# Kernel optimization log

Hardware: AMD Instinct MI355X
Metric: run time of the kernel (lower is better)

The kernel has to match this reference:

```python
import jax, jax.numpy as jnp
import numpy as np

V = 50257   # vocab
P = 2048    # max positions
D = 768     # hidden
H = 12      # heads
F = 3072    # 4*D ffn
NL = 12     # layers
L = 2048    # seq len
EPS = 1e-5


def setup_inputs() -> dict:
    key = jax.random.key(0)
    ks = jax.random.split(key, 12)
    r = lambda k, shp: jax.random.normal(k, shp, jnp.float32) * 0.02
    return dict(
        input_ids=jax.random.randint(ks[0], (1, L), 0, V, dtype=jnp.int32),
        attention_mask=jnp.ones((1, L), jnp.int32),
        wte=r(ks[1], (V, D)),
        wpe=r(ks[2], (P, D)),
        lnf_w=jnp.ones((D,), jnp.float32),
        lnf_b=jnp.zeros((D,), jnp.float32),
        ln1_w=jnp.ones((NL, D), jnp.float32),
        ln1_b=jnp.zeros((NL, D), jnp.float32),
        qw=r(ks[3], (NL, D, D)),
        kw=r(ks[4], (NL, D, D)),
        vw=r(ks[5], (NL, D, D)),
        ow=r(ks[6], (NL, D, D)),
        ob=jnp.zeros((NL, D), jnp.float32),
        ln2_w=jnp.ones((NL, D), jnp.float32),
        ln2_b=jnp.zeros((NL, D), jnp.float32),
        fcw=r(ks[7], (NL, D, F)),
        fcb=jnp.zeros((NL, F), jnp.float32),
        pw=r(ks[8], (NL, F, D)),
        pb=jnp.zeros((NL, D), jnp.float32),
    )


def _ln(x, w, b):
    mu = jnp.mean(x, -1, keepdims=True)
    var = jnp.mean((x - mu) ** 2, -1, keepdims=True)
    return (x - mu) * jax.lax.rsqrt(var + EPS) * w + b


def reference(input_ids, attention_mask, wte, wpe, lnf_w, lnf_b,
              ln1_w, ln1_b, qw, kw, vw, ow, ob, ln2_w, ln2_b,
              fcw, fcb, pw, pb):
    ids = input_ids.reshape(-1, input_ids.shape[-1])          # [1, L]
    pos = jnp.cumsum(attention_mask, -1) - 1
    pos = jnp.where(attention_mask == 0, 1, pos)
    h = (wte[ids] + wpe[pos])[0]                               # [L, D]

    key_valid = attention_mask[0] > 0                          # actual_length mask
    mask = jnp.tril(jnp.ones((L, L), bool)) & key_valid[None, :]  # causal+pad
    dh = D // H

    def layer(h, p):
        l1w, l1b, Wq, Wk, Wv, Wo, bo, l2w, l2b, Wf, bf, Wp, bp = p
        x = _ln(h, l1w, l1b)
        q = (x @ Wq).reshape(L, H, dh)
        k = (x @ Wk).reshape(L, H, dh)
        v = (x @ Wv).reshape(L, H, dh)
        # GPT-Neo attention: NO 1/sqrt(dh) scaling
        scores = jnp.einsum('qhd,khd->hqk', q, k)
        scores = jnp.where(mask[None], scores, jnp.float32(-1e9))
        attn = jax.nn.softmax(scores, axis=-1)
        ctx = jnp.einsum('hqk,khd->qhd', attn, v).reshape(L, D)
        h = h + ctx @ Wo + bo
        y = _ln(h, l2w, l2b)
        h = h + jax.nn.gelu(y @ Wf + bf, approximate=True) @ Wp + bp
        return h, None

    h, _ = jax.lax.scan(layer, h, (ln1_w, ln1_b, qw, kw, vw, ow, ob,
                                   ln2_w, ln2_b, fcw, fcb, pw, pb))
    return _ln(h[None, :, :], lnf_w, lnf_b)                    # [1, L, D]
```

## Files before the change

kernel.cpp:

```cpp
#include <hip/hip_runtime.h>
#include <hip/hip_bf16.h>
#include <math.h>
#include <stdint.h>

#define L 2048
#define D 768
#define H 12
#define DH 64
#define F 3072
#define NL 12
#define QKVN 2304

typedef __attribute__((ext_vector_type(8))) short bf16x8;
typedef __attribute__((ext_vector_type(4))) float f32x4;

__device__ __forceinline__ ushort f2bf(float x) {
    union { float f; uint32_t u; } c; c.f = x;
    uint32_t r = c.u + 0x7FFFu + ((c.u >> 16) & 1u);
    return (ushort)(r >> 16);
}

__device__ __forceinline__ uint32_t cvt_pk_bf16(float lo, float hi) {
    uint32_t r;
    asm("v_cvt_pk_bf16_f32 %0, %1, %2" : "=v"(r) : "v"(lo), "v"(hi));
    return r;
}

__device__ __forceinline__ bf16x8 ldfrag(const ushort* p) {
    ushort4 lo = *(const ushort4*)(p);
    ushort4 hi = *(const ushort4*)(p + 16);
    bf16x8 f;
    f[0] = (short)lo.x; f[1] = (short)lo.y; f[2] = (short)lo.z; f[3] = (short)lo.w;
    f[4] = (short)hi.x; f[5] = (short)hi.y; f[6] = (short)hi.z; f[7] = (short)hi.w;
    return f;
}

__device__ __forceinline__ float gelu_tanh(float x) {
    float c = 0.7978845608028654f;
    float inner = c * (x + 0.044715f * x * x * x);
    return 0.5f * x * (1.0f + tanhf(inner));
}

__global__ void pos_kernel(const int* __restrict__ mask, int* __restrict__ pos) {
    __shared__ int sm[L];
    for (int i = threadIdx.x; i < L; i += blockDim.x) sm[i] = mask[i];
    __syncthreads();
    int t = blockIdx.x * blockDim.x + threadIdx.x;
    if (t < L) {
        int s = 0;
        for (int j = 0; j <= t; ++j) s += sm[j];
        int p = s - 1;
        if (sm[t] == 0) p = 1;
        pos[t] = p;
    }
}

__global__ void maskb_kernel(const int* __restrict__ mask, float* __restrict__ mb) {
    int i = blockIdx.x * blockDim.x + threadIdx.x;
    if (i < L) mb[i] = mask[i] ? 0.f : -1e9f;
}

__global__ __launch_bounds__(256) void embed_kernel(const int* __restrict__ ids,
                                                    const int* __restrict__ pos,
                                                    const float* __restrict__ wte,
                                                    const float* __restrict__ wpe,
                                                    float* __restrict__ h) {
    int t = blockIdx.x;
    int id = ids[t];
    int p = pos[t];
    const float* we = wte + (size_t)id * D;
    const float* wp = wpe + (size_t)p * D;
    float* hr = h + (size_t)t * D;
#pragma unroll
    for (int i = 0; i < 3; ++i) {
        int d = threadIdx.x + i * 256;
        hr[d] = we[d] + wp[d];
    }
}

template <bool OUTBF>
__global__ __launch_bounds__(256) void ln_kernel(const float* __restrict__ in,
                                                 const float* __restrict__ w,
                                                 const float* __restrict__ b,
                                                 float* __restrict__ outF,
                                                 ushort* __restrict__ outB) {
    __shared__ float red[2][4];
    int row = blockIdx.x;
    const float* x = in + (size_t)row * D;
    int t = threadIdx.x;
    float v0 = x[t], v1 = x[t + 256], v2 = x[t + 512];
    float s = v0 + v1 + v2;
    float ss = v0 * v0 + v1 * v1 + v2 * v2;
#pragma unroll
    for (int o = 32; o; o >>= 1) {
        s += __shfl_xor(s, o);
        ss += __shfl_xor(ss, o);
    }
    int wave = t >> 6;
    if ((t & 63) == 0) { red[0][wave] = s; red[1][wave] = ss; }
    __syncthreads();
    s = red[0][0] + red[0][1] + red[0][2] + red[0][3];
    ss = red[1][0] + red[1][1] + red[1][2] + red[1][3];
    float mean = s * (1.f / D);
    float var = ss * (1.f / D) - mean * mean;
    float rstd = rsqrtf(var + 1e-5f);
#pragma unroll
    for (int i = 0; i < 3; ++i) {
        int d = t + i * 256;
        float vv = (i == 0) ? v0 : (i == 1) ? v1 : v2;
        float y = (vv - mean) * rstd * w[d] + b[d];
        if (OUTBF) outB[(size_t)row * D + d] = f2bf(y);
        else       outF[(size_t)row * D + d] = y;
    }
}

template <int S, bool OUTBF>
__global__ __launch_bounds__(256) void redln_kernel(const float* __restrict__ part,
                                                    const float* __restrict__ bias,
                                                    float* __restrict__ h,
                                                    const float* __restrict__ lnw,
                                                    const float* __restrict__ lnb,
                                                    ushort* __restrict__ outB,
                                                    float* __restrict__ outF) {
    __shared__ float red[2][4];
    int row = blockIdx.x;
    int t = threadIdx.x;
    float v[3];
    float s = 0.f, ss = 0.f;
#pragma unroll
    for (int i = 0; i < 3; ++i) {
        int d = t + i * 256;
        float x = h[(size_t)row * D + d] + bias[d];
#pragma unroll
        for (int sp = 0; sp < S; ++sp)
            x += part[((size_t)sp * L + row) * D + d];
        v[i] = x;
        h[(size_t)row * D + d] = x;
        s += x;
        ss += x * x;
    }
#pragma unroll
    for (int o = 32; o; o >>= 1) {
        s += __shfl_xor(s, o);
        ss += __shfl_xor(ss, o);
    }
    int wave = t >> 6;
    if ((t & 63) == 0) { red[0][wave] = s; red[1][wave] = ss; }
    __syncthreads();
    s = red[0][0] + red[0][1] + red[0][2] + red[0][3];
    ss = red[1][0] + red[1][1] + red[1][2] + red[1][3];
    float mean = s * (1.f / D);
    float var = ss * (1.f / D) - mean * mean;
    float rstd = rsqrtf(var + 1e-5f);
#pragma unroll
    for (int i = 0; i < 3; ++i) {
        int d = t + i * 256;
        float y = (v[i] - mean) * rstd * lnw[d] + lnb[d];
        if (OUTBF) outB[(size_t)row * D + d] = f2bf(y);
        else       outF[(size_t)row * D + d] = y;
    }
}

__global__ __launch_bounds__(256) void tcast_f32(const float* __restrict__ in,
                                                 ushort* __restrict__ out,
                                                 int K, int N,
                                                 size_t inStride, size_t outStride) {
    in += blockIdx.z * inStride;
    out += blockIdx.z * outStride;
    __shared__ float tile[64][65];
    int k0 = blockIdx.y * 64, n0 = blockIdx.x * 64;
    int t = threadIdx.x;
    int cl = t & 63, rg = t >> 6;
#pragma unroll
    for (int i = 0; i < 16; ++i) {
        int r = rg + 4 * i;
        tile[r][cl] = in[(size_t)(k0 + r) * N + n0 + cl];
    }
    __syncthreads();
#pragma unroll
    for (int i = 0; i < 16; ++i) {
        int r = rg + 4 * i;
        out[(size_t)(n0 + r) * K + k0 + cl] = f2bf(tile[cl][r]);
    }
}

template <int ACT, bool OUTBF, int SPLITK, bool VSPLIT>
__global__ __launch_bounds__(256) void gemm_bf16(const ushort* __restrict__ A,
                                                 const ushort* __restrict__ Bt,
                                                 const float* __restrict__ bias,
                                                 const float* __restrict__ resid,
                                                 float* __restrict__ outF,
                                                 ushort* __restrict__ outB,
                                                 float* __restrict__ pout,
                                                 ushort* __restrict__ vTout,
                                                 int M, int N, int K) {
    __shared__ __align__(16) char lds[32768];
    const int tid = threadIdx.x;
    const int lane = tid & 63, w = tid >> 6;
    const int wr = w >> 1, wc = w & 1;
    const int bm = blockIdx.y * 128, bn = blockIdx.x * 128;
    const int l15 = lane & 15, l4 = lane >> 4;
    const int srow = tid >> 2, c = tid & 3;
    const int blo = (c & 1) * 32 + (c >> 1) * 8;
    const int kLen = K / SPLITK;
    const int kStart = (SPLITK > 1) ? blockIdx.z * kLen : 0;

    const int sxor = (srow & 3) << 4;
    const int wo0 = srow * 64 + (blo ^ sxor);
    const int wo1 = srow * 64 + ((blo + 16) ^ sxor);
    const int rxor = (l4 * 16) ^ ((l15 & 3) << 4);
    const int aBase = (wr * 64 + l15) * 64 + rxor;
    const int bBase = (wc * 64 + l15) * 64 + rxor;

    f32x4 acc[4][4];
#pragma unroll
    for (int m = 0; m < 4; ++m)
#pragma unroll
        for (int n = 0; n < 4; ++n)
            acc[m][n] = (f32x4){0.f, 0.f, 0.f, 0.f};

    const ushort* Ag = A + (size_t)(bm + srow) * K + kStart + c * 8;
    const ushort* Ag2 = Ag + (size_t)64 * K;
    const ushort* Bg = Bt + (size_t)(bn + srow) * K + kStart + c * 8;
    const ushort* Bg2 = Bg + (size_t)64 * K;

    uint4 a0 = *(const uint4*)(Ag);
    uint4 a1 = *(const uint4*)(Ag2);
    uint4 b0 = *(const uint4*)(Bg);
    uint4 b1 = *(const uint4*)(Bg2);

    for (int k0 = 0; k0 < kLen; k0 += 32) {
        char* Ab = lds + ((k0 >> 5) & 1) * 16384;
        char* Bb = Ab + 8192;
        uint2 t0, t1;
        t0.x = a0.x; t0.y = a0.y; t1.x = a0.z; t1.y = a0.w;
        *(uint2*)(Ab + wo0) = t0;
        *(uint2*)(Ab + wo1) = t1;
        t0.x = a1.x; t0.y = a1.y; t1.x = a1.z; t1.y = a1.w;
        *(uint2*)(Ab + wo0 + 4096) = t0;
        *(uint2*)(Ab + wo1 + 4096) = t1;
        t0.x = b0.x; t0.y = b0.y; t1.x = b0.z; t1.y = b0.w;
        *(uint2*)(Bb + wo0) = t0;
        *(uint2*)(Bb + wo1) = t1;
        t0.x = b1.x; t0.y = b1.y; t1.x = b1.z; t1.y = b1.w;
        *(uint2*)(Bb + wo0 + 4096) = t0;
        *(uint2*)(Bb + wo1 + 4096) = t1;
        __syncthreads();
        if (k0 + 32 < kLen) {
            a0 = *(const uint4*)(Ag + k0 + 32);
            a1 = *(const uint4*)(Ag2 + k0 + 32);
            b0 = *(const uint4*)(Bg + k0 + 32);
            b1 = *(const uint4*)(Bg2 + k0 + 32);
        }
        bf16x8 af[4], bfv[4];
#pragma unroll
        for (int m = 0; m < 4; ++m)
            af[m] = *(const bf16x8*)(Ab + aBase + m * 1024);
#pragma unroll
        for (int n = 0; n < 4; ++n)
            bfv[n] = *(const bf16x8*)(Bb + bBase + n * 1024);
#pragma unroll
        for (int m = 0; m < 4; ++m)
#pragma unroll
            for (int n = 0; n < 4; ++n)
                acc[m][n] = __builtin_amdgcn_mfma_f32_16x16x32_bf16(af[m], bfv[n], acc[m][n], 0, 0, 0);
    }

    if (SPLITK > 1) {
        const size_t sb = (size_t)blockIdx.z * M;
#pragma unroll
        for (int m = 0; m < 4; ++m)
#pragma unroll
            for (int n = 0; n < 4; ++n) {
                int col = bn + wc * 64 + n * 16 + l15;
#pragma unroll
                for (int r = 0; r < 4; ++r) {
                    int row = bm + wr * 64 + m * 16 + l4 * 4 + r;
                    pout[(sb + row) * N + col] = acc[m][n][r];
                }
            }
    } else {
#pragma unroll
        for (int m = 0; m < 4; ++m)
#pragma unroll
            for (int n = 0; n < 4; ++n) {
                int col = bn + wc * 64 + n * 16 + l15;
                int row0 = bm + wr * 64 + m * 16 + l4 * 4;
                if (VSPLIT && col >= 2 * D) {
                    ushort4 pk;
                    pk.x = f2bf(acc[m][n][0]);
                    pk.y = f2bf(acc[m][n][1]);
                    pk.z = f2bf(acc[m][n][2]);
                    pk.w = f2bf(acc[m][n][3]);
                    *(ushort4*)(vTout + (size_t)(col - 2 * D) * L + row0) = pk;
                } else {
#pragma unroll
                    for (int r = 0; r < 4; ++r) {
                        int row = row0 + r;
                        float v = acc[m][n][r];
                        if (bias) v += bias[col];
                        if (ACT == 1) v = gelu_tanh(v);
                        if (resid) v += resid[(size_t)row * N + col];
                        if (OUTBF) outB[(size_t)row * N + col] = f2bf(v);
                        else       outF[(size_t)row * N + col] = v;
                    }
                }
            }
    }
}

template <int NS>
__global__ __launch_bounds__(256) void attn_kernel(const ushort* __restrict__ qkv,
                                                   const ushort* __restrict__ vT,
                                                   const float* __restrict__ maskb,
                                                   float* __restrict__ po,
                                                   float* __restrict__ pm,
                                                   float* __restrict__ pl) {
    __shared__ __align__(16) char Kl[2][8192];
    __shared__ __align__(16) char Vl[2][8192];
    __shared__ float Ml[2][64];
    const int hh = blockIdx.y;
    const int sp = blockIdx.z;
    const int q0 = ((int)gridDim.x - 1 - (int)blockIdx.x) * 64;
    const int tid = threadIdx.x;
    const int lane = tid & 63, w = tid >> 6;
    const int l15 = lane & 15, l4 = lane >> 4;
    const int qg = q0 + w * 16 + l15;
    const int qmin = q0 + w * 16;

    const int nt = q0 / 64 + 1;
    const int chunk = (nt + NS - 1) / NS;
    const int it0 = sp * chunk;
    int it1 = it0 + chunk;
    if (it1 > nt) it1 = nt;

    f32x4 o[4];
#pragma unroll
    for (int i = 0; i < 4; ++i) o[i] = (f32x4){0.f, 0.f, 0.f, 0.f};
    float mrun = -1e30f, lrun = 0.f;

    if (it0 < it1) {
        bf16x8 qf[2];
#pragma unroll
        for (int ks = 0; ks < 2; ++ks)
            qf[ks] = ldfrag(qkv + (size_t)qg * QKVN + hh * 64 + ks * 32 + l4 * 4);

        const int srow = tid >> 2, c = tid & 3;
        const int blo = (c & 1) * 32 + (c >> 1) * 8;
        const int swz = (srow & 7) << 4;
        const int rb = srow * 128;
        const int lo4 = blo & 15;
        const int s0 = rb + (((blo)      & 0x70) ^ swz) + lo4;
        const int s1 = rb + (((blo + 16) & 0x70) ^ swz) + lo4;
        const int s2 = rb + (((blo + 64) & 0x70) ^ swz) + lo4;
        const int s3 = rb + (((blo + 80) & 0x70) ^ swz) + lo4;
        const int fxor = (l15 & 7) << 4;

        const ushort* Ksrc = qkv + (size_t)srow * QKVN + D + hh * 64 + c * 8;
        const ushort* Vsrc = vT + (size_t)(hh * 64 + srow) * L + c * 8;

        uint4 ka, kb, va, vb;
        float mv = 0.f;
        {
            const size_t koff = (size_t)(it0 * 64) * QKVN;
            ka = *(const uint4*)(Ksrc + koff);
            kb = *(const uint4*)(Ksrc + koff + 32);
            va = *(const uint4*)(Vsrc + it0 * 64);
            vb = *(const uint4*)(Vsrc + it0 * 64 + 32);
            if (tid < 64) mv = maskb[it0 * 64 + tid];
        }

        for (int it = it0; it < it1; ++it) {
            const int kv0 = it * 64;
            const int b = it & 1;
            {
                char* Kb = Kl[b];
                char* Vb = Vl[b];
                uint2 t0, t1;
                t0.x = ka.x; t0.y = ka.y; t1.x = ka.z; t1.y = ka.w;
                *(uint2*)(Kb + s0) = t0;
                *(uint2*)(Kb + s1) = t1;
                t0.x = kb.x; t0.y = kb.y; t1.x = kb.z; t1.y = kb.w;
                *(uint2*)(Kb + s2) = t0;
                *(uint2*)(Kb + s3) = t1;
                t0.x = va.x; t0.y = va.y; t1.x = va.z; t1.y = va.w;
                *(uint2*)(Vb + s0) = t0;
                *(uint2*)(Vb + s1) = t1;
                t0.x = vb.x; t0.y = vb.y; t1.x = vb.z; t1.y = vb.w;
                *(uint2*)(Vb + s2) = t0;
                *(uint2*)(Vb + s3) = t1;
                if (tid < 64) Ml[b][tid] = mv;
            }
            __syncthreads();
            if (it + 1 < it1) {
                const size_t koff = (size_t)(kv0 + 64) * QKVN;
                ka = *(const uint4*)(Ksrc + koff);
                kb = *(const uint4*)(Ksrc + koff + 32);
                va = *(const uint4*)(Vsrc + kv0 + 64);
                vb = *(const uint4*)(Vsrc + kv0 + 96);
                if (tid < 64) mv = maskb[kv0 + 64 + tid];
            }

            const char* Kb = Kl[b];
            const char* Vb = Vl[b];

            f32x4 st[4];
#pragma unroll
            for (int m = 0; m < 4; ++m) st[m] = (f32x4){0.f, 0.f, 0.f, 0.f};
#pragma unroll
            for (int m = 0; m < 4; ++m)
#pragma unroll
                for (int ks = 0; ks < 2; ++ks) {
                    bf16x8 kf = *(const bf16x8*)(Kb + (m * 16 + l15) * 128 +
                                                 ((ks * 64 + l4 * 16) ^ fxor));
                    st[m] = __builtin_amdgcn_mfma_f32_16x16x32_bf16(kf, qf[ks], st[m], 0, 0, 0);
                }

            float p[4][4];
            float tmax = -1e30f;
            const bool full = (kv0 + 63 <= qmin);
            if (full) {
#pragma unroll
                for (int m = 0; m < 4; ++m)
#pragma unroll
                    for (int r = 0; r < 4; ++r) {
                        int kl = m * 16 + l4 * 4 + r;
                        float s = st[m][r] + Ml[b][kl];
                        p[m][r] = s;
                        tmax = fmaxf(tmax, s);
                    }
            } else {
#pragma unroll
                for (int m = 0; m < 4; ++m)
#pragma unroll
                    for (int r = 0; r < 4; ++r) {
                        int kl = m * 16 + l4 * 4 + r;
                        float s = st[m][r] + Ml[b][kl];
                        if (kv0 + kl > qg) s = -1e30f;
                        p[m][r] = s;
                        tmax = fmaxf(tmax, s);
                    }
            }
            tmax = fmaxf(tmax, __shfl_xor(tmax, 16));
            tmax = fmaxf(tmax, __shfl_xor(tmax, 32));
            const bool noresc = __all(tmax <= mrun);
            float mnew = noresc ? mrun : fmaxf(mrun, tmax);
            float scale = noresc ? 1.f : __expf(mrun - mnew);
            float ts = 0.f;
#pragma unroll
            for (int m = 0; m < 4; ++m)
#pragma unroll
                for (int r = 0; r < 4; ++r) {
                    float e = __expf(p[m][r] - mnew);
                    p[m][r] = e;
                    ts += e;
                }
            ts += __shfl_xor(ts, 16);
            ts += __shfl_xor(ts, 32);
            lrun = lrun * scale + ts;
            mrun = mnew;

            bf16x8 pf[2];
#pragma unroll
            for (int g = 0; g < 2; ++g) {
                union { bf16x8 v; uint32_t d[4]; } pu;
                pu.d[0] = cvt_pk_bf16(p[2 * g][0], p[2 * g][1]);
                pu.d[1] = cvt_pk_bf16(p[2 * g][2], p[2 * g][3]);
                pu.d[2] = cvt_pk_bf16(p[2 * g + 1][0], p[2 * g + 1][1]);
                pu.d[3] = cvt_pk_bf16(p[2 * g + 1][2], p[2 * g + 1][3]);
                pf[g] = pu.v;
            }
            if (!noresc) {
#pragma unroll
                for (int i = 0; i < 4; ++i) {
                    o[i][0] *= scale; o[i][1] *= scale; o[i][2] *= scale; o[i][3] *= scale;
                }
            }
#pragma unroll
            for (int dhb = 0; dhb < 4; ++dhb)
#pragma unroll
                for (int g = 0; g < 2; ++g) {
                    bf16x8 vf = *(const bf16x8*)(Vb + (dhb * 16 + l15) * 128 +
                                                 ((g * 64 + l4 * 16) ^ fxor));
                    o[dhb] = __builtin_amdgcn_mfma_f32_16x16x32_bf16(vf, pf[g], o[dhb], 0, 0, 0);
                }
        }
    }

    const size_t pb = (size_t)(sp * H + hh) * L + qg;
    if (l4 == 0) { pm[pb] = mrun; pl[pb] = lrun; }
    float* op = po + pb * 64;
#pragma unroll
    for (int dhb = 0; dhb < 4; ++dhb)
        *(f32x4*)(op + dhb * 16 + l4 * 4) = o[dhb];
}

template <int NS>
__global__ __launch_bounds__(256) void attn_combine(const float* __restrict__ po,
                                                    const float* __restrict__ pm,
                                                    const float* __restrict__ pl,
                                                    ushort* __restrict__ ctx) {
    const int hh = blockIdx.y;
    const int q = blockIdx.x * 64 + (threadIdx.x >> 2);
    const int d0 = (threadIdx.x & 3) * 16;
    size_t idx[NS];
    float mm = -1e30f;
#pragma unroll
    for (int s = 0; s < NS; ++s) {
        idx[s] = (size_t)(s * H + hh) * L + q;
        mm = fmaxf(mm, pm[idx[s]]);
    }
    float e[NS];
    float l = 0.f;
#pragma unroll
    for (int s = 0; s < NS; ++s) {
        e[s] = __expf(pm[idx[s]] - mm);
        l += pl[idx[s]] * e[s];
    }
    float rinv = 1.0f / l;
    ushort* cp = ctx + (size_t)q * D + hh * 64 + d0;
#pragma unroll
    for (int j = 0; j < 16; j += 4) {
        float acc[4] = {0.f, 0.f, 0.f, 0.f};
#pragma unroll
        for (int s = 0; s < NS; ++s) {
            const float* op = po + idx[s] * 64 + d0 + j;
            float4 v = *(const float4*)op;
            acc[0] += v.x * e[s];
            acc[1] += v.y * e[s];
            acc[2] += v.z * e[s];
            acc[3] += v.w * e[s];
        }
        ushort4 pk;
        pk.x = f2bf(acc[0] * rinv);
        pk.y = f2bf(acc[1] * rinv);
        pk.z = f2bf(acc[2] * rinv);
        pk.w = f2bf(acc[3] * rinv);
        *(ushort4*)(cp + j) = pk;
    }
}

extern "C" void kernel_launch(void* const* d_in, const int* in_sizes, int n_in,
                              void* d_out, int out_size, void* d_ws, size_t ws_size,
                              hipStream_t stream) {
    const int* ids = (const int*)d_in[0];
    const int* amask = (const int*)d_in[1];
    const float* wte = (const float*)d_in[2];
    const float* wpe = (const float*)d_in[3];
    const float* lnf_w = (const float*)d_in[4];
    const float* lnf_b = (const float*)d_in[5];
    const float* ln1_w = (const float*)d_in[6];
    const float* ln1_b = (const float*)d_in[7];
    const float* qw = (const float*)d_in[8];
    const float* kw = (const float*)d_in[9];
    const float* vw = (const float*)d_in[10];
    const float* ow = (const float*)d_in[11];
    const float* ob = (const float*)d_in[12];
    const float* ln2_w = (const float*)d_in[13];
    const float* ln2_b = (const float*)d_in[14];
    const float* fcw = (const float*)d_in[15];
    const float* fcb = (const float*)d_in[16];
    const float* pw = (const float*)d_in[17];
    const float* pb = (const float*)d_in[18];

    char* p = (char*)d_ws;
    auto take = [&](size_t bytes) -> char* {
        char* r = p;
        p += (bytes + 4095) & ~(size_t)4095;
        return r;
    };
    ushort* wqkvT = (ushort*)take((size_t)NL * QKVN * D * 2);
    ushort* woT   = (ushort*)take((size_t)NL * D * D * 2);
    ushort* fcwT  = (ushort*)take((size_t)NL * F * D * 2);
    ushort* pwT   = (ushort*)take((size_t)NL * D * F * 2);
    float*  h     = (float*)take((size_t)L * D * 4);
    ushort* xb    = (ushort*)take((size_t)L * D * 2);
    ushort* qkvb  = (ushort*)take((size_t)L * QKVN * 2);
    ushort* vTb   = (ushort*)take((size_t)D * L * 2);
    ushort* ctxb  = (ushort*)take((size_t)L * D * 2);
    ushort* f1b   = (ushort*)take((size_t)L * F * 2);
    float*  pk    = (float*)take((size_t)4 * L * D * 4);
    float*  po    = (float*)take((size_t)2 * H * L * 64 * 4);
    float*  pm    = (float*)take((size_t)2 * H * L * 4);
    float*  pl    = (float*)take((size_t)2 * H * L * 4);
    float*  mb    = (float*)take(L * 4);
    int*    pos   = (int*)take(L * 4);

    pos_kernel<<<8, 256, 0, stream>>>(amask, pos);
    maskb_kernel<<<8, 256, 0, stream>>>(amask, mb);
    embed_kernel<<<L, 256, 0, stream>>>(ids, pos, wte, wpe, h);

    tcast_f32<<<dim3(12, 12, NL), 256, 0, stream>>>(qw, wqkvT, D, D,
                                                    (size_t)D * D, (size_t)QKVN * D);
    tcast_f32<<<dim3(12, 12, NL), 256, 0, stream>>>(kw, wqkvT + (size_t)D * D, D, D,
                                                    (size_t)D * D, (size_t)QKVN * D);
    tcast_f32<<<dim3(12, 12, NL), 256, 0, stream>>>(vw, wqkvT + (size_t)2 * D * D, D, D,
                                                    (size_t)D * D, (size_t)QKVN * D);
    tcast_f32<<<dim3(12, 12, NL), 256, 0, stream>>>(ow, woT, D, D,
                                                    (size_t)D * D, (size_t)D * D);
    tcast_f32<<<dim3(48, 12, NL), 256, 0, stream>>>(fcw, fcwT, D, F,
                                                    (size_t)D * F, (size_t)F * D);
    tcast_f32<<<dim3(12, 48, NL), 256, 0, stream>>>(pw, pwT, F, D,
                                                    (size_t)F * D, (size_t)D * F);

    ln_kernel<true><<<L, 256, 0, stream>>>(h, ln1_w, ln1_b, nullptr, xb);

    for (int l = 0; l < NL; ++l) {
        gemm_bf16<0, true, 1, true><<<dim3(QKVN / 128, L / 128), 256, 0, stream>>>(
            xb, wqkvT + (size_t)l * QKVN * D, nullptr, nullptr, nullptr, qkvb, nullptr,
            vTb, L, QKVN, D);
        attn_kernel<2><<<dim3(L / 64, H, 2), 256, 0, stream>>>(qkvb, vTb, mb,
                                                               po, pm, pl);
        attn_combine<2><<<dim3(L / 64, H), 256, 0, stream>>>(po, pm, pl, ctxb);
        gemm_bf16<0, true, 4, false><<<dim3(D / 128, L / 128, 4), 256, 0, stream>>>(
            ctxb, woT + (size_t)l * D * D, nullptr, nullptr, nullptr, nullptr, pk,
            nullptr, L, D, D);
        redln_kernel<4, true><<<L, 256, 0, stream>>>(
            pk, ob + l * D, h, ln2_w + l * D, ln2_b + l * D, xb, nullptr);
        gemm_bf16<1, true, 1, false><<<dim3(F / 128, L / 128), 256, 0, stream>>>(
            xb, fcwT + (size_t)l * F * D, fcb + l * F, nullptr, nullptr, f1b, nullptr,
            nullptr, L, F, D);
        gemm_bf16<0, true, 4, false><<<dim3(D / 128, L / 128, 4), 256, 0, stream>>>(
            f1b, pwT + (size_t)l * D * F, nullptr, nullptr, nullptr, nullptr, pk,
            nullptr, L, D, F);
        if (l < NL - 1) {
            redln_kernel<4, true><<<L, 256, 0, stream>>>(
                pk, pb + l * D, h, ln1_w + (l + 1) * D, ln1_b + (l + 1) * D, xb, nullptr);
        } else {
            redln_kernel<4, false><<<L, 256, 0, stream>>>(
                pk, pb + l * D, h, lnf_w, lnf_b, nullptr, (float*)d_out);
        }
    }
}
```

Measured before the change: 1.825 ms.

## Deepen GEMM global prefetch to two register stages with unrolled k-loop

The GEMM main loop is unrolled by two k-steps, with two sets of prefetch registers holding global loads two tiles ahead instead of one. This gives each global load more time to complete behind MFMA work and removes the per-iteration LDS buffer-index arithmetic. In exchange it uses more registers, which can lower occupancy, and it assumes kLen is a multiple of 64. Without a second barrier before each buffer is rewritten, the hazard on reuse of the LDS buffers may also change.

```diff
diff --git a/kernel.cpp b/kernel.cpp
--- a/kernel.cpp
+++ b/kernel.cpp
@@ -224,47 +224,77 @@
     const ushort* Bg = Bt + (size_t)(bn + srow) * K + kStart + c * 8;
     const ushort* Bg2 = Bg + (size_t)64 * K;
 
-    uint4 a0 = *(const uint4*)(Ag);
-    uint4 a1 = *(const uint4*)(Ag2);
-    uint4 b0 = *(const uint4*)(Bg);
-    uint4 b1 = *(const uint4*)(Bg2);
-
-    for (int k0 = 0; k0 < kLen; k0 += 32) {
-        char* Ab = lds + ((k0 >> 5) & 1) * 16384;
-        char* Bb = Ab + 8192;
-        uint2 t0, t1;
-        t0.x = a0.x; t0.y = a0.y; t1.x = a0.z; t1.y = a0.w;
-        *(uint2*)(Ab + wo0) = t0;
-        *(uint2*)(Ab + wo1) = t1;
-        t0.x = a1.x; t0.y = a1.y; t1.x = a1.z; t1.y = a1.w;
-        *(uint2*)(Ab + wo0 + 4096) = t0;
-        *(uint2*)(Ab + wo1 + 4096) = t1;
-        t0.x = b0.x; t0.y = b0.y; t1.x = b0.z; t1.y = b0.w;
-        *(uint2*)(Bb + wo0) = t0;
-        *(uint2*)(Bb + wo1) = t1;
-        t0.x = b1.x; t0.y = b1.y; t1.x = b1.z; t1.y = b1.w;
-        *(uint2*)(Bb + wo0 + 4096) = t0;
-        *(uint2*)(Bb + wo1 + 4096) = t1;
+    uint4 xa0, xa1, xb0, xb1;
+    uint4 ya0, ya1, yb0, yb1;
+    xa0 = *(const uint4*)(Ag);
+    xa1 = *(const uint4*)(Ag2);
+    xb0 = *(const uint4*)(Bg);
+    xb1 = *(const uint4*)(Bg2);
+    ya0 = *(const uint4*)(Ag + 32);
+    ya1 = *(const uint4*)(Ag2 + 32);
+    yb0 = *(const uint4*)(Bg + 32);
+    yb1 = *(const uint4*)(Bg2 + 32);
+
+#define GSTAGE_WRITE(BUF, A0, A1, B0, B1)                     \
+    {                                                          \
+        char* Ab_ = lds + (BUF) * 16384;                       \
+        char* Bb_ = Ab_ + 8192;                                \
+        uint2 t0, t1;                                          \
+        t0.x = A0.x; t0.y = A0.y; t1.x = A0.z; t1.y = A0.w;    \
+        *(uint2*)(Ab_ + wo0) = t0;                             \
+        *(uint2*)(Ab_ + wo1) = t1;                             \
+        t0.x = A1.x; t0.y = A1.y; t1.x = A1.z; t1.y = A1.w;    \
+        *(uint2*)(Ab_ + wo0 + 4096) = t0;                      \
+        *(uint2*)(Ab_ + wo1 + 4096) = t1;                      \
+        t0.x = B0.x; t0.y = B0.y; t1.x = B0.z; t1.y = B0.w;    \
+        *(uint2*)(Bb_ + wo0) = t0;                             \
+        *(uint2*)(Bb_ + wo1) = t1;                             \
+        t0.x = B1.x; t0.y = B1.y; t1.x = B1.z; t1.y = B1.w;    \
+        *(uint2*)(Bb_ + wo0 + 4096) = t0;                      \
+        *(uint2*)(Bb_ + wo1 + 4096) = t1;                      \
+    }
+
+#define GCOMPUTE(BUF)                                                     \
+    {                                                                      \
+        char* Ab_ = lds + (BUF) * 16384;                                   \
+        char* Bb_ = Ab_ + 8192;                                            \
+        bf16x8 af[4], bfv[4];                                              \
+        _Pragma("unroll")                                                  \
+        for (int m = 0; m < 4; ++m)                                        \
+            af[m] = *(const bf16x8*)(Ab_ + aBase + m * 1024);              \
+        _Pragma("unroll")                                                  \
+        for (int n = 0; n < 4; ++n)                                        \
+            bfv[n] = *(const bf16x8*)(Bb_ + bBase + n * 1024);             \
+        _Pragma("unroll")                                                  \
+        for (int m = 0; m < 4; ++m)                                        \
+            _Pragma("unroll")                                              \
+            for (int n = 0; n < 4; ++n)                                    \
+                acc[m][n] = __builtin_amdgcn_mfma_f32_16x16x32_bf16(       \
+                    af[m], bfv[n], acc[m][n], 0, 0, 0);                    \
+    }
+
+    for (int k0 = 0; k0 < kLen; k0 += 64) {
+        GSTAGE_WRITE(0, xa0, xa1, xb0, xb1);
         __syncthreads();
-        if (k0 + 32 < kLen) {
-            a0 = *(const uint4*)(Ag + k0 + 32);
-            a1 = *(const uint4*)(Ag2 + k0 + 32);
-            b0 = *(const uint4*)(Bg + k0 + 32);
-            b1 = *(const uint4*)(Bg2 + k0 + 32);
+        if (k0 + 64 < kLen) {
+            xa0 = *(const uint4*)(Ag + k0 + 64);
+            xa1 = *(const uint4*)(Ag2 + k0 + 64);
+            xb0 = *(const uint4*)(Bg + k0 + 64);
+            xb1 = *(const uint4*)(Bg2 + k0 + 64);
         }
-        bf16x8 af[4], bfv[4];
-#pragma unroll
-        for (int m = 0; m < 4; ++m)
-            af[m] = *(const bf16x8*)(Ab + aBase + m * 1024);
-#pragma unroll
-        for (int n = 0; n < 4; ++n)
-            bfv[n] = *(const bf16x8*)(Bb + bBase + n * 1024);
-#pragma unroll
-        for (int m = 0; m < 4; ++m)
-#pragma unroll
-            for (int n = 0; n < 4; ++n)
-                acc[m][n] = __builtin_amdgcn_mfma_f32_16x16x32_bf16(af[m], bfv[n], acc[m][n], 0, 0, 0);
-    }
+        GCOMPUTE(0);
+        GSTAGE_WRITE(1, ya0, ya1, yb0, yb1);
+        __syncthreads();
+        if (k0 + 96 < kLen) {
+            ya0 = *(const uint4*)(Ag + k0 + 96);
+            ya1 = *(const uint4*)(Ag2 + k0 + 96);
+            yb0 = *(const uint4*)(Bg + k0 + 96);
+            yb1 = *(const uint4*)(Bg2 + k0 + 96);
+        }
+        GCOMPUTE(1);
+    }
+#undef GSTAGE_WRITE
+#undef GCOMPUTE
 
     if (SPLITK > 1) {
         const size_t sb = (size_t)blockIdx.z * M;
```

Result: no change. 1.808 ms (-0.9%).
